# Optimization experiments

Hardware: AMD Instinct MI355X
Metric: run time of the kernel (lower is better)

Reference implementation:

```python
import jax, jax.numpy as jnp
import numpy as np

N = 100000      # nodes
E = 3200000     # edges (avg degree 32, undirected)
FIN = 256
FOUT = 256
K = 4


def setup_inputs() -> dict:
    key = jax.random.key(0)
    k1, k2, k3 = jax.random.split(key, 3)
    x = jax.random.normal(k1, (N, FIN), dtype=jnp.float32)
    edge_index = jax.random.randint(k2, (2, E), 0, N, dtype=jnp.int32)
    stdv = 1.0 / np.sqrt(FIN * K)
    # K per-hop dense projection weights, uniform(-stdv, stdv) as in reset_parameters
    weights = jax.random.uniform(k3, (K, FIN, FOUT), dtype=jnp.float32,
                                 minval=-stdv, maxval=stdv)
    return {"x": x, "edge_index": edge_index, "weights": weights}


def reference(x, edge_index, weights):
    # edge_index -> symmetric adjacency S (from_edgelist builds an undirected graph):
    # spmm(S, z)[i] = sum over neighbors j of z[j]; scatter-add both directions.
    src, dst = edge_index[0], edge_index[1]

    def spmm(z):
        out = jnp.zeros_like(z).at[dst].add(z[src])
        return out.at[src].add(z[dst])

    zs = [x]
    for _ in range(1, weights.shape[0]):
        x = spmm(x)           # [N, Fin] k-hop diffused features
        zs.append(x)
    # sum_k zs[k] @ weights[k]  -> [N, Fout]
    return jnp.einsum('knf,kfo->no', jnp.stack(zs), weights)
```

## Files before the change

kernel.cpp:

```cpp
#include <hip/hip_runtime.h>
#include <hip/hip_bf16.h>


#define NNODES 100000
#define NEDGES 3200000
#define FOUTF  256
#define MPAD   100096
#define MTILES 782
#define NB     782
#define NCHUNK 1024
#define CHUNK  3125

typedef __attribute__((ext_vector_type(4))) int   i32x4;
typedef __attribute__((ext_vector_type(4))) float f32x4;

__device__ __forceinline__ void async_ld16(const void* g, void* l) {
  __builtin_amdgcn_global_load_lds(
      (const __attribute__((address_space(1))) unsigned int*)g,
      (__attribute__((address_space(3))) unsigned int*)l, 16, 0, 0);
}


__global__ __launch_bounds__(256)
void chunk_count_kernel(const int* __restrict__ ei, int* __restrict__ cntg) {
  __shared__ int h[NB];
  for (int i = threadIdx.x; i < NB; i += 256) h[i] = 0;
  __syncthreads();
  const int e0 = blockIdx.x * CHUNK;
  const int e1 = (e0 + CHUNK < NEDGES) ? e0 + CHUNK : NEDGES;
  for (int e = e0 + threadIdx.x; e < e1; e += 256) {
    int s = ei[e];
    int d = ei[NEDGES + e];
    atomicAdd(&h[d >> 7], 1);
    atomicAdd(&h[s >> 7], 1);
  }
  __syncthreads();
  for (int i = threadIdx.x; i < NB; i += 256)
    cntg[blockIdx.x * NB + i] = h[i];
}

__global__ __launch_bounds__(256)
void scan_chunks_kernel(int* __restrict__ cntg, int* __restrict__ tot) {
  __shared__ int ws2[4];
  const int v = blockIdx.x;
  const int t = threadIdx.x, lane = t & 63, wv = t >> 6;
  int c[4];
  int sum = 0;
  #pragma unroll
  for (int i = 0; i < 4; ++i) { c[i] = cntg[(4 * t + i) * NB + v]; sum += c[i]; }
  int s = sum;
  #pragma unroll
  for (int off = 1; off < 64; off <<= 1) {
    int tmp = __shfl_up(s, off, 64);
    if (lane >= off) s += tmp;
  }
  if (lane == 63) ws2[wv] = s;
  __syncthreads();
  int wpre = 0;
  #pragma unroll
  for (int k = 0; k < 4; ++k) wpre += (k < wv) ? ws2[k] : 0;
  int run = wpre + s - sum;
  #pragma unroll
  for (int i = 0; i < 4; ++i) { int tmp = c[i]; cntg[(4 * t + i) * NB + v] = run; run += tmp; }
  if (t == 255) tot[v] = wpre + s;
}

__global__ __launch_bounds__(1024)
void base_scan_kernel(const int* __restrict__ tot, int* __restrict__ bbase) {
  __shared__ int ws[16];
  int t = threadIdx.x, lane = t & 63, wv = t >> 6;
  int v = (t < NB) ? tot[t] : 0;
  int s = v;
  #pragma unroll
  for (int off = 1; off < 64; off <<= 1) {
    int tmp = __shfl_up(s, off, 64);
    if (lane >= off) s += tmp;
  }
  if (lane == 63) ws[wv] = s;
  __syncthreads();
  if (t == 0) {
    int run = 0;
    #pragma unroll
    for (int k = 0; k < 16; ++k) { int tmp = ws[k]; ws[k] = run; run += tmp; }
  }
  __syncthreads();
  int excl = s + ws[wv] - v;
  if (t < NB) bbase[t] = excl;
  if (t == NB) bbase[NB] = excl;
}

__global__ __launch_bounds__(256)
void fill_kernel(const int* __restrict__ ei, const int* __restrict__ cntg,
                 const int* __restrict__ bbase, unsigned int* __restrict__ binned) {
  __shared__ int cur[NB];
  const int b = blockIdx.x;
  for (int i = threadIdx.x; i < NB; i += 256)
    cur[i] = bbase[i] + cntg[b * NB + i];
  __syncthreads();
  const int e0 = b * CHUNK;
  const int e1 = (e0 + CHUNK < NEDGES) ? e0 + CHUNK : NEDGES;
  for (int e = e0 + threadIdx.x; e < e1; e += 256) {
    int s = ei[e];
    int d = ei[NEDGES + e];
    int p = atomicAdd(&cur[d >> 7], 1);
    binned[p] = ((unsigned int)(d & 127) << 17) | (unsigned int)s;
    int q = atomicAdd(&cur[s >> 7], 1);
    binned[q] = ((unsigned int)(s & 127) << 17) | (unsigned int)d;
  }
}

__global__ __launch_bounds__(256)
void bucket_csr_kernel(const unsigned int* __restrict__ binned,
                       const int* __restrict__ bbase,
                       int* __restrict__ row_ptr, int* __restrict__ adj) {
  __shared__ int cnt[128];
  __shared__ int cur[128];
  const int b = blockIdx.x;
  const int node0 = b << 7;
  const int base = bbase[b];
  const int end = bbase[b + 1];
  const int tid = threadIdx.x;
  if (tid < 128) cnt[tid] = 0;
  __syncthreads();
  for (int i = base + tid; i < end; i += 256) {
    unsigned int v = binned[i];
    atomicAdd(&cnt[v >> 17], 1);
  }
  __syncthreads();
  if (tid < 128) {
    int ex = 0;
    #pragma unroll 8
    for (int j = 0; j < 128; ++j) {
      int c = cnt[j];
      ex += (j < tid) ? c : 0;
    }
    int node = node0 + tid;
    if (node < NNODES) row_ptr[node] = base + ex;
    cur[tid] = base + ex;
  }
  if (tid == 0 && b == NB - 1) row_ptr[NNODES] = end;
  __syncthreads();
  for (int i = base + tid; i < end; i += 256) {
    unsigned int v = binned[i];
    int nbr = (int)(v & 0x1FFFFu);
    int p = atomicAdd(&cur[v >> 17], 1);
    adj[p] = nbr << 8;
  }
}


__global__ __launch_bounds__(256)
void convert_x_kernel(const float* __restrict__ x,
                      unsigned char* __restrict__ g0,
                      float* __restrict__ sc0) {
  const int row = (blockIdx.x * 256 + threadIdx.x) >> 6;
  const int lane = threadIdx.x & 63;
  if (row >= NNODES) return;
  float4 xv = *(const float4*)&x[(size_t)row * 256 + (lane << 2)];

  float m = fmaxf(fmaxf(fabsf(xv.x), fabsf(xv.y)), fmaxf(fabsf(xv.z), fabsf(xv.w)));
  #pragma unroll
  for (int i = 1; i < 64; i <<= 1) m = fmaxf(m, __shfl_xor(m, i, 64));
  float inv = (m > 0.f) ? 127.f / m : 0.f;
  int q0 = (int)__builtin_rintf(xv.x * inv);
  int q1 = (int)__builtin_rintf(xv.y * inv);
  int q2 = (int)__builtin_rintf(xv.z * inv);
  int q3 = (int)__builtin_rintf(xv.w * inv);
  *(unsigned int*)(g0 + (size_t)row * 256 + (lane << 2)) =
      ((unsigned)q0 & 255u) | (((unsigned)q1 & 255u) << 8) |
      (((unsigned)q2 & 255u) << 16) | (((unsigned)q3 & 255u) << 24);
  if (lane == 0) sc0[row] = m * (1.f / 127.f);
}

__global__ __launch_bounds__(256)
void wmax_kernel(const float* __restrict__ w, unsigned int* __restrict__ dWmax) {
  __shared__ float red[4];
  const int k = blockIdx.x >> 6;
  const int chunk = blockIdx.x & 63;
  const float* wk = w + (size_t)k * 65536 + chunk * 1024;
  float m = 0.f;
  #pragma unroll
  for (int i = 0; i < 4; ++i) m = fmaxf(m, fabsf(wk[threadIdx.x + i * 256]));
  #pragma unroll
  for (int i = 1; i < 64; i <<= 1) m = fmaxf(m, __shfl_xor(m, i, 64));
  if ((threadIdx.x & 63) == 0) red[threadIdx.x >> 6] = m;
  __syncthreads();
  if (threadIdx.x == 0) {
    m = fmaxf(fmaxf(red[0], red[1]), fmaxf(red[2], red[3]));
    atomicMax(&dWmax[k], __float_as_uint(m));
  }
}

__global__ void quantw_kernel(const float* __restrict__ w,
                              const unsigned int* __restrict__ dWmax,
                              signed char* __restrict__ W8) {
  int idx = blockIdx.x * 256 + threadIdx.x;
  int k = idx >> 16, f = (idx >> 8) & 255, o = idx & 255;
  float mx = __uint_as_float(dWmax[k]);
  float inv = (mx > 0.f) ? 127.f / mx : 0.f;
  W8[(size_t)k * 65536 + o * 256 + f] = (signed char)(int)__builtin_rintf(w[idx] * inv);
}


#define DECQ(vv, ss)                                        \
  { acc0 += (ss) * (float)((vv) & 255u);                    \
    acc1 += (ss) * (float)(((vv) >> 8) & 255u);             \
    acc2 += (ss) * (float)(((vv) >> 16) & 255u);            \
    acc3 += (ss) * (float)((vv) >> 24);                     \
    ssum += (ss); }

__global__ __launch_bounds__(256)
void spmm_q8_kernel(const unsigned char* __restrict__ gin,
                    const float* __restrict__ sin,
                    unsigned char* __restrict__ gout,
                    float* __restrict__ sout,
                    const int* __restrict__ row_ptr,
                    const int* __restrict__ adjb) {
  const int wid = __builtin_amdgcn_readfirstlane((blockIdx.x * 256 + threadIdx.x) >> 6);
  const int lane = threadIdx.x & 63;
  if (wid >= NNODES) return;
  const int beg = row_ptr[wid];
  const int end = row_ptr[wid + 1];
  const int lb = lane << 2;
  const char* scb = (const char*)sin;

  float acc0 = 0.f, acc1 = 0.f, acc2 = 0.f, acc3 = 0.f, ssum = 0.f;
  int j = beg;
  for (; j + 4 <= end; j += 4) {
    int o0 = adjb[j + 0], o1 = adjb[j + 1], o2 = adjb[j + 2], o3 = adjb[j + 3];
    float s0 = *(const float*)(scb + (o0 >> 6));
    float s1 = *(const float*)(scb + (o1 >> 6));
    float s2 = *(const float*)(scb + (o2 >> 6));
    float s3 = *(const float*)(scb + (o3 >> 6));
    unsigned int v0 = *(const unsigned int*)(gin + o0 + lb) ^ 0x80808080u;
    unsigned int v1 = *(const unsigned int*)(gin + o1 + lb) ^ 0x80808080u;
    unsigned int v2 = *(const unsigned int*)(gin + o2 + lb) ^ 0x80808080u;
    unsigned int v3 = *(const unsigned int*)(gin + o3 + lb) ^ 0x80808080u;
    DECQ(v0, s0); DECQ(v1, s1); DECQ(v2, s2); DECQ(v3, s3);
  }
  for (; j < end; ++j) {
    int o = adjb[j];
    float s = *(const float*)(scb + (o >> 6));
    unsigned int v = *(const unsigned int*)(gin + o + lb) ^ 0x80808080u;
    DECQ(v, s);
  }

  const float bias = 128.f * ssum;
  const float a0 = acc0 - bias;
  const float a1 = acc1 - bias;
  const float a2 = acc2 - bias;
  const float a3 = acc3 - bias;

  float m = fmaxf(fmaxf(fabsf(a0), fabsf(a1)), fmaxf(fabsf(a2), fabsf(a3)));
  #pragma unroll
  for (int i = 1; i < 64; i <<= 1) m = fmaxf(m, __shfl_xor(m, i, 64));
  float inv = (m > 0.f) ? 127.f / m : 0.f;
  int q0 = (int)__builtin_rintf(a0 * inv);
  int q1 = (int)__builtin_rintf(a1 * inv);
  int q2 = (int)__builtin_rintf(a2 * inv);
  int q3 = (int)__builtin_rintf(a3 * inv);
  *(unsigned int*)(gout + (size_t)wid * 256 + lb) =
      ((unsigned)q0 & 255u) | (((unsigned)q1 & 255u) << 8) |
      (((unsigned)q2 & 255u) << 16) | (((unsigned)q3 & 255u) << 24);
  if (lane == 0) sout[wid] = m * (1.f / 127.f);
}


__global__ __launch_bounds__(512)
void gemm_i8_kernel(const unsigned char* __restrict__ q0p,
                    const unsigned char* __restrict__ q1p,
                    const unsigned char* __restrict__ q2p,
                    const unsigned char* __restrict__ q3p,
                    const float* __restrict__ s0p,
                    const float* __restrict__ s1p,
                    const float* __restrict__ s2p,
                    const float* __restrict__ s3p,
                    const signed char* __restrict__ W8,
                    const unsigned int* __restrict__ dWmax,
                    float* __restrict__ C) {
  __shared__ __align__(16) unsigned char smem[49152];
  unsigned char* As = smem;
  unsigned char* Bs = smem + 16384;
  const int tid = threadIdx.x;
  const int lane = tid & 63;
  const int wave = tid >> 6;
  const int wr = wave >> 2;
  const int wc = wave & 3;
  const int rowA_base = blockIdx.x * 128;

  const unsigned char* qs[4] = {q0p, q1p, q2p, q3p};
  const float* scs[4] = {s0p, s1p, s2p, s3p};

  f32x4 accf[4][4] = {};

  #pragma unroll
  for (int k = 0; k < 4; ++k) {
    const unsigned char* Qk = qs[k];
    const signed char* Wk = W8 + (size_t)k * 65536;
    i32x4 acci[4][4] = {};
    #pragma unroll
    for (int kc = 0; kc < 2; ++kc) {
      __syncthreads();
      #pragma unroll
      for (int i = 0; i < 2; ++i) {
        int slot = tid + 512 * i;
        int row = slot >> 3;
        int col = ((slot & 7) << 4) ^ ((row & 7) << 4);
        async_ld16(Qk + (size_t)(rowA_base + row) * 256 + kc * 128 + col,
                   &As[slot * 16]);
      }
      #pragma unroll
      for (int i = 0; i < 4; ++i) {
        int slot = tid + 512 * i;
        int row = slot >> 3;
        int col = ((slot & 7) << 4) ^ ((row & 7) << 4);
        async_ld16(Wk + (size_t)row * 256 + kc * 128 + col, &Bs[slot * 16]);
      }
      __syncthreads();
      #pragma unroll
      for (int kk = 0; kk < 2; ++kk) {
        const int kb = kk * 64 + ((lane >> 4) << 4);
        i32x4 a[4], b[4];
        #pragma unroll
        for (int m = 0; m < 4; ++m) {
          int row = wr * 64 + m * 16 + (lane & 15);
          a[m] = *(const i32x4*)&As[row * 128 + (kb ^ ((row & 7) << 4))];
        }
        #pragma unroll
        for (int n = 0; n < 4; ++n) {
          int row = wc * 64 + n * 16 + (lane & 15);
          b[n] = *(const i32x4*)&Bs[row * 128 + (kb ^ ((row & 7) << 4))];
        }
        #pragma unroll
        for (int m = 0; m < 4; ++m) {
          #pragma unroll
          for (int n = 0; n < 4; ++n)
            acci[m][n] = __builtin_amdgcn_mfma_i32_16x16x64_i8(a[m], b[n], acci[m][n], 0, 0, 0);
        }
      }
    }
    const float dWk = __uint_as_float(dWmax[k]) * (1.f / 127.f);
    const float* sk = scs[k];
    #pragma unroll
    for (int m = 0; m < 4; ++m) {
      #pragma unroll
      for (int j = 0; j < 4; ++j) {
        int r = rowA_base + wr * 64 + ((lane >> 4) << 2) + m * 16 + j;
        float s = sk[r] * dWk;
        #pragma unroll
        for (int n = 0; n < 4; ++n)
          accf[m][n][j] += s * (float)acci[m][n][j];
      }
    }
  }

  __syncthreads();
  float* myCs = (float*)smem + wave * 1056;
  #pragma unroll
  for (int m = 0; m < 4; ++m) {
    #pragma unroll
    for (int n = 0; n < 4; ++n) {
      #pragma unroll
      for (int j = 0; j < 4; ++j)
        myCs[(((lane >> 4) << 2) | j) * 66 + (lane & 15) + n * 16] = accf[m][n][j];
    }
    #pragma unroll
    for (int it = 0; it < 4; ++it) {
      int row = it * 4 + (lane >> 4);
      f32x4 v = *(const f32x4*)&myCs[row * 66 + ((lane & 15) << 2)];
      int r = rowA_base + wr * 64 + m * 16 + row;
      if (r < NNODES)
        *(f32x4*)&C[(size_t)r * FOUTF + wc * 64 + ((lane & 15) << 2)] = v;
    }
  }
}


extern "C" void kernel_launch(void* const* d_in, const int* in_sizes, int n_in,
                              void* d_out, int out_size, void* d_ws, size_t ws_size,
                              hipStream_t stream) {
  (void)in_sizes; (void)n_in; (void)out_size; (void)ws_size;
  const float* x  = (const float*)d_in[0];
  const int*   ei = (const int*)d_in[1];
  const float* w  = (const float*)d_in[2];
  float* out = (float*)d_out;

  char* ws = (char*)d_ws;
  size_t off = 0;
  auto carve = [&](size_t bytes) -> void* {
    void* p = ws + off;
    off = (off + bytes + 255) & ~(size_t)255;
    return p;
  };
  unsigned char* gA = (unsigned char*)carve((size_t)MPAD * 256);
  unsigned char* gB = (unsigned char*)carve((size_t)MPAD * 256);
  unsigned char* gC = (unsigned char*)carve((size_t)MPAD * 256);
  unsigned char* gD = (unsigned char*)carve((size_t)MPAD * 256);
  float* scA        = (float*)carve((size_t)MPAD * 4);
  float* scB        = (float*)carve((size_t)MPAD * 4);
  float* scC        = (float*)carve((size_t)MPAD * 4);
  float* scD        = (float*)carve((size_t)MPAD * 4);
  signed char* W8   = (signed char*)carve((size_t)4 * 65536);
  unsigned int* dWmax = (unsigned int*)carve(4 * 4);
  int* row_ptr      = (int*)carve((size_t)(NNODES + 1) * 4);
  int* adj          = (int*)carve((size_t)2 * NEDGES * 4);
  int* cntg         = (int*)carve((size_t)NCHUNK * NB * 4);
  int* tot          = (int*)carve((size_t)NB * 4);
  int* bbase        = (int*)carve((size_t)(NB + 1) * 4);
  unsigned int* binned = (unsigned int*)gD;

  hipMemsetAsync(dWmax, 0, 16, stream);

  chunk_count_kernel<<<NCHUNK, 256, 0, stream>>>(ei, cntg);
  scan_chunks_kernel<<<NB, 256, 0, stream>>>(cntg, tot);
  base_scan_kernel<<<1, 1024, 0, stream>>>(tot, bbase);
  fill_kernel<<<NCHUNK, 256, 0, stream>>>(ei, cntg, bbase, binned);
  bucket_csr_kernel<<<NB, 256, 0, stream>>>(binned, bbase, row_ptr, adj);

  convert_x_kernel<<<25000, 256, 0, stream>>>(x, gA, scA);
  wmax_kernel<<<256, 256, 0, stream>>>(w, dWmax);
  quantw_kernel<<<1024, 256, 0, stream>>>(w, dWmax, W8);

  spmm_q8_kernel<<<25000, 256, 0, stream>>>(gA, scA, gB, scB, row_ptr, adj);
  spmm_q8_kernel<<<25000, 256, 0, stream>>>(gB, scB, gC, scC, row_ptr, adj);
  spmm_q8_kernel<<<25000, 256, 0, stream>>>(gC, scC, gD, scD, row_ptr, adj);

  gemm_i8_kernel<<<MTILES, 512, 0, stream>>>(gA, gB, gC, gD, scA, scB, scC, scD,
                                             W8, dWmax, out);
}
```

Baseline: 938.9 us.

## Fuse front kernels, sort adjacency per row, use persistent spmm grid

Merges x quantization, edge chunk counting and weight max reduction into one launch with block-range dispatch. Adds a per-row sort of adjacency entries by high bits of the byte offset so neighbor gathers walk memory in coarse order. Switches the spmm kernels to a grid-stride persistent layout of 2048 blocks. Together these aim to cut launch overhead and improve gather locality, at the cost of an extra sort pass over the adjacency.

```diff
diff --git a/kernel.cpp b/kernel.cpp
--- a/kernel.cpp
+++ b/kernel.cpp
@@ -20,24 +20,63 @@
       (__attribute__((address_space(3))) unsigned int*)l, 16, 0, 0);
 }
 
-
-__global__ __launch_bounds__(256)
-void chunk_count_kernel(const int* __restrict__ ei, int* __restrict__ cntg) {
+__global__ __launch_bounds__(256)
+void front_kernel(const float* __restrict__ x,
+                  unsigned char* __restrict__ g0, float* __restrict__ sc0,
+                  const int* __restrict__ ei, int* __restrict__ cntg,
+                  const float* __restrict__ w, unsigned int* __restrict__ dWmax) {
   __shared__ int h[NB];
-  for (int i = threadIdx.x; i < NB; i += 256) h[i] = 0;
-  __syncthreads();
-  const int e0 = blockIdx.x * CHUNK;
-  const int e1 = (e0 + CHUNK < NEDGES) ? e0 + CHUNK : NEDGES;
-  for (int e = e0 + threadIdx.x; e < e1; e += 256) {
-    int s = ei[e];
-    int d = ei[NEDGES + e];
-    atomicAdd(&h[d >> 7], 1);
-    atomicAdd(&h[s >> 7], 1);
-  }
-  __syncthreads();
-  for (int i = threadIdx.x; i < NB; i += 256)
-    cntg[blockIdx.x * NB + i] = h[i];
-}
+  const int bid = blockIdx.x;
+  if (bid < 25000) {
+    const int row = (bid * 256 + threadIdx.x) >> 6;
+    const int lane = threadIdx.x & 63;
+    if (row >= NNODES) return;
+    float4 xv = *(const float4*)&x[(size_t)row * 256 + (lane << 2)];
+    float m = fmaxf(fmaxf(fabsf(xv.x), fabsf(xv.y)), fmaxf(fabsf(xv.z), fabsf(xv.w)));
+    #pragma unroll
+    for (int i = 1; i < 64; i <<= 1) m = fmaxf(m, __shfl_xor(m, i, 64));
+    float inv = (m > 0.f) ? 127.f / m : 0.f;
+    int q0 = (int)__builtin_rintf(xv.x * inv);
+    int q1 = (int)__builtin_rintf(xv.y * inv);
+    int q2 = (int)__builtin_rintf(xv.z * inv);
+    int q3 = (int)__builtin_rintf(xv.w * inv);
+    *(unsigned int*)(g0 + (size_t)row * 256 + (lane << 2)) =
+        ((unsigned)q0 & 255u) | (((unsigned)q1 & 255u) << 8) |
+        (((unsigned)q2 & 255u) << 16) | (((unsigned)q3 & 255u) << 24);
+    if (lane == 0) sc0[row] = m * (1.f / 127.f);
+  } else if (bid < 26024) {
+    const int b = bid - 25000;
+    for (int i = threadIdx.x; i < NB; i += 256) h[i] = 0;
+    __syncthreads();
+    const int e0 = b * CHUNK;
+    const int e1 = (e0 + CHUNK < NEDGES) ? e0 + CHUNK : NEDGES;
+    for (int e = e0 + threadIdx.x; e < e1; e += 256) {
+      int s = ei[e];
+      int d = ei[NEDGES + e];
+      atomicAdd(&h[d >> 7], 1);
+      atomicAdd(&h[s >> 7], 1);
+    }
+    __syncthreads();
+    for (int i = threadIdx.x; i < NB; i += 256)
+      cntg[b * NB + i] = h[i];
+  } else {
+    const int b = bid - 26024;
+    const int k = b >> 6;
+    const int chunk = b & 63;
+    const float* wk = w + (size_t)k * 65536 + chunk * 1024;
+    float m = 0.f;
+    #pragma unroll
+    for (int i = 0; i < 4; ++i) m = fmaxf(m, fabsf(wk[threadIdx.x + i * 256]));
+    #pragma unroll
+    for (int i = 1; i < 64; i <<= 1) m = fmaxf(m, __shfl_xor(m, i, 64));
+    if (threadIdx.x == 0) h[0] = 0;
+    __syncthreads();
+    if ((threadIdx.x & 63) == 0) atomicMax(&h[0], __float_as_int(m));
+    __syncthreads();
+    if (threadIdx.x == 0) atomicMax(&dWmax[k], (unsigned int)h[0]);
+  }
+}
+
 
 __global__ __launch_bounds__(256)
 void scan_chunks_kernel(int* __restrict__ cntg, int* __restrict__ tot) {
@@ -148,46 +187,43 @@
   }
 }
 
-
-__global__ __launch_bounds__(256)
-void convert_x_kernel(const float* __restrict__ x,
-                      unsigned char* __restrict__ g0,
-                      float* __restrict__ sc0) {
-  const int row = (blockIdx.x * 256 + threadIdx.x) >> 6;
+__global__ __launch_bounds__(256)
+void sort_adj_kernel(const int* __restrict__ row_ptr, int* __restrict__ adj) {
+  __shared__ int cnt[4][32];
+  __shared__ int cur[4][32];
+  const int wv = threadIdx.x >> 6;
   const int lane = threadIdx.x & 63;
-  if (row >= NNODES) return;
-  float4 xv = *(const float4*)&x[(size_t)row * 256 + (lane << 2)];
-
-  float m = fmaxf(fmaxf(fabsf(xv.x), fabsf(xv.y)), fmaxf(fabsf(xv.z), fabsf(xv.w)));
-  #pragma unroll
-  for (int i = 1; i < 64; i <<= 1) m = fmaxf(m, __shfl_xor(m, i, 64));
-  float inv = (m > 0.f) ? 127.f / m : 0.f;
-  int q0 = (int)__builtin_rintf(xv.x * inv);
-  int q1 = (int)__builtin_rintf(xv.y * inv);
-  int q2 = (int)__builtin_rintf(xv.z * inv);
-  int q3 = (int)__builtin_rintf(xv.w * inv);
-  *(unsigned int*)(g0 + (size_t)row * 256 + (lane << 2)) =
-      ((unsigned)q0 & 255u) | (((unsigned)q1 & 255u) << 8) |
-      (((unsigned)q2 & 255u) << 16) | (((unsigned)q3 & 255u) << 24);
-  if (lane == 0) sc0[row] = m * (1.f / 127.f);
-}
-
-__global__ __launch_bounds__(256)
-void wmax_kernel(const float* __restrict__ w, unsigned int* __restrict__ dWmax) {
-  __shared__ float red[4];
-  const int k = blockIdx.x >> 6;
-  const int chunk = blockIdx.x & 63;
-  const float* wk = w + (size_t)k * 65536 + chunk * 1024;
-  float m = 0.f;
-  #pragma unroll
-  for (int i = 0; i < 4; ++i) m = fmaxf(m, fabsf(wk[threadIdx.x + i * 256]));
-  #pragma unroll
-  for (int i = 1; i < 64; i <<= 1) m = fmaxf(m, __shfl_xor(m, i, 64));
-  if ((threadIdx.x & 63) == 0) red[threadIdx.x >> 6] = m;
-  __syncthreads();
-  if (threadIdx.x == 0) {
-    m = fmaxf(fmaxf(red[0], red[1]), fmaxf(red[2], red[3]));
-    atomicMax(&dWmax[k], __float_as_uint(m));
+  const int wid = blockIdx.x * 4 + wv;
+  if (wid >= NNODES) return;
+  const int beg = row_ptr[wid];
+  const int deg = row_ptr[wid + 1] - beg;
+  if (deg > 256) return;
+  if (lane < 32) cnt[wv][lane] = 0;
+  int v[4];
+  #pragma unroll
+  for (int i = 0; i < 4; ++i) {
+    int idx = lane + 64 * i;
+    v[i] = (idx < deg) ? adj[beg + idx] : -1;
+  }
+  #pragma unroll
+  for (int i = 0; i < 4; ++i)
+    if (v[i] >= 0) atomicAdd(&cnt[wv][((unsigned)v[i]) >> 20], 1);
+  if (lane < 32) {
+    int c = cnt[wv][lane];
+    int s = c;
+    #pragma unroll
+    for (int off = 1; off < 32; off <<= 1) {
+      int tmp = __shfl_up(s, off, 32);
+      if ((lane & 31) >= off) s += tmp;
+    }
+    cur[wv][lane] = s - c;
+  }
+  #pragma unroll
+  for (int i = 0; i < 4; ++i) {
+    if (v[i] >= 0) {
+      int pos = atomicAdd(&cur[wv][((unsigned)v[i]) >> 20], 1);
+      adj[beg + pos] = v[i];
+    }
   }
 }
 
@@ -216,53 +252,57 @@
                     float* __restrict__ sout,
                     const int* __restrict__ row_ptr,
                     const int* __restrict__ adjb) {
-  const int wid = __builtin_amdgcn_readfirstlane((blockIdx.x * 256 + threadIdx.x) >> 6);
+  const int wv = threadIdx.x >> 6;
   const int lane = threadIdx.x & 63;
-  if (wid >= NNODES) return;
-  const int beg = row_ptr[wid];
-  const int end = row_ptr[wid + 1];
+  const int wbase = blockIdx.x * 4 + wv;
   const int lb = lane << 2;
   const char* scb = (const char*)sin;
 
-  float acc0 = 0.f, acc1 = 0.f, acc2 = 0.f, acc3 = 0.f, ssum = 0.f;
-  int j = beg;
-  for (; j + 4 <= end; j += 4) {
-    int o0 = adjb[j + 0], o1 = adjb[j + 1], o2 = adjb[j + 2], o3 = adjb[j + 3];
-    float s0 = *(const float*)(scb + (o0 >> 6));
-    float s1 = *(const float*)(scb + (o1 >> 6));
-    float s2 = *(const float*)(scb + (o2 >> 6));
-    float s3 = *(const float*)(scb + (o3 >> 6));
-    unsigned int v0 = *(const unsigned int*)(gin + o0 + lb) ^ 0x80808080u;
-    unsigned int v1 = *(const unsigned int*)(gin + o1 + lb) ^ 0x80808080u;
-    unsigned int v2 = *(const unsigned int*)(gin + o2 + lb) ^ 0x80808080u;
-    unsigned int v3 = *(const unsigned int*)(gin + o3 + lb) ^ 0x80808080u;
-    DECQ(v0, s0); DECQ(v1, s1); DECQ(v2, s2); DECQ(v3, s3);
-  }
-  for (; j < end; ++j) {
-    int o = adjb[j];
-    float s = *(const float*)(scb + (o >> 6));
-    unsigned int v = *(const unsigned int*)(gin + o + lb) ^ 0x80808080u;
-    DECQ(v, s);
-  }
-
-  const float bias = 128.f * ssum;
-  const float a0 = acc0 - bias;
-  const float a1 = acc1 - bias;
-  const float a2 = acc2 - bias;
-  const float a3 = acc3 - bias;
-
-  float m = fmaxf(fmaxf(fabsf(a0), fabsf(a1)), fmaxf(fabsf(a2), fabsf(a3)));
-  #pragma unroll
-  for (int i = 1; i < 64; i <<= 1) m = fmaxf(m, __shfl_xor(m, i, 64));
-  float inv = (m > 0.f) ? 127.f / m : 0.f;
-  int q0 = (int)__builtin_rintf(a0 * inv);
-  int q1 = (int)__builtin_rintf(a1 * inv);
-  int q2 = (int)__builtin_rintf(a2 * inv);
-  int q3 = (int)__builtin_rintf(a3 * inv);
-  *(unsigned int*)(gout + (size_t)wid * 256 + lb) =
-      ((unsigned)q0 & 255u) | (((unsigned)q1 & 255u) << 8) |
-      (((unsigned)q2 & 255u) << 16) | (((unsigned)q3 & 255u) << 24);
-  if (lane == 0) sout[wid] = m * (1.f / 127.f);
+  for (int wid0 = wbase; wid0 < NNODES; wid0 += 8192) {
+    const int wid = __builtin_amdgcn_readfirstlane(wid0);
+    const int beg = row_ptr[wid];
+    const int end = row_ptr[wid + 1];
+
+    float acc0 = 0.f, acc1 = 0.f, acc2 = 0.f, acc3 = 0.f, ssum = 0.f;
+    int j = beg;
+    for (; j + 4 <= end; j += 4) {
+      int o0 = adjb[j + 0], o1 = adjb[j + 1], o2 = adjb[j + 2], o3 = adjb[j + 3];
+      float s0 = *(const float*)(scb + (o0 >> 6));
+      float s1 = *(const float*)(scb + (o1 >> 6));
+      float s2 = *(const float*)(scb + (o2 >> 6));
+      float s3 = *(const float*)(scb + (o3 >> 6));
+      unsigned int v0 = *(const unsigned int*)(gin + o0 + lb) ^ 0x80808080u;
+      unsigned int v1 = *(const unsigned int*)(gin + o1 + lb) ^ 0x80808080u;
+      unsigned int v2 = *(const unsigned int*)(gin + o2 + lb) ^ 0x80808080u;
+      unsigned int v3 = *(const unsigned int*)(gin + o3 + lb) ^ 0x80808080u;
+      DECQ(v0, s0); DECQ(v1, s1); DECQ(v2, s2); DECQ(v3, s3);
+    }
+    for (; j < end; ++j) {
+      int o = adjb[j];
+      float s = *(const float*)(scb + (o >> 6));
+      unsigned int v = *(const unsigned int*)(gin + o + lb) ^ 0x80808080u;
+      DECQ(v, s);
+    }
+
+    const float bias = 128.f * ssum;
+    const float a0 = acc0 - bias;
+    const float a1 = acc1 - bias;
+    const float a2 = acc2 - bias;
+    const float a3 = acc3 - bias;
+
+    float m = fmaxf(fmaxf(fabsf(a0), fabsf(a1)), fmaxf(fabsf(a2), fabsf(a3)));
+    #pragma unroll
+    for (int i = 1; i < 64; i <<= 1) m = fmaxf(m, __shfl_xor(m, i, 64));
+    float inv = (m > 0.f) ? 127.f / m : 0.f;
+    int q0 = (int)__builtin_rintf(a0 * inv);
+    int q1 = (int)__builtin_rintf(a1 * inv);
+    int q2 = (int)__builtin_rintf(a2 * inv);
+    int q3 = (int)__builtin_rintf(a3 * inv);
+    *(unsigned int*)(gout + (size_t)wid * 256 + lb) =
+        ((unsigned)q0 & 255u) | (((unsigned)q1 & 255u) << 8) |
+        (((unsigned)q2 & 255u) << 16) | (((unsigned)q3 & 255u) << 24);
+    if (lane == 0) sout[wid] = m * (1.f / 127.f);
+  }
 }
 
 
@@ -411,19 +451,17 @@
 
   hipMemsetAsync(dWmax, 0, 16, stream);
 
-  chunk_count_kernel<<<NCHUNK, 256, 0, stream>>>(ei, cntg);
+  front_kernel<<<26280, 256, 0, stream>>>(x, gA, scA, ei, cntg, w, dWmax);
   scan_chunks_kernel<<<NB, 256, 0, stream>>>(cntg, tot);
   base_scan_kernel<<<1, 1024, 0, stream>>>(tot, bbase);
   fill_kernel<<<NCHUNK, 256, 0, stream>>>(ei, cntg, bbase, binned);
   bucket_csr_kernel<<<NB, 256, 0, stream>>>(binned, bbase, row_ptr, adj);
-
-  convert_x_kernel<<<25000, 256, 0, stream>>>(x, gA, scA);
-  wmax_kernel<<<256, 256, 0, stream>>>(w, dWmax);
+  sort_adj_kernel<<<25000, 256, 0, stream>>>(row_ptr, adj);
   quantw_kernel<<<1024, 256, 0, stream>>>(w, dWmax, W8);
 
-  spmm_q8_kernel<<<25000, 256, 0, stream>>>(gA, scA, gB, scB, row_ptr, adj);
-  spmm_q8_kernel<<<25000, 256, 0, stream>>>(gB, scB, gC, scC, row_ptr, adj);
-  spmm_q8_kernel<<<25000, 256, 0, stream>>>(gC, scC, gD, scD, row_ptr, adj);
+  spmm_q8_kernel<<<2048, 256, 0, stream>>>(gA, scA, gB, scB, row_ptr, adj);
+  spmm_q8_kernel<<<2048, 256, 0, stream>>>(gB, scB, gC, scC, row_ptr, adj);
+  spmm_q8_kernel<<<2048, 256, 0, stream>>>(gC, scC, gD, scD, row_ptr, adj);
 
   gemm_i8_kernel<<<MTILES, 512, 0, stream>>>(gA, gB, gC, gD, scA, scB, scC, scD,
                                              W8, dWmax, out);
```

After: 1.005 ms. +7.1%, slower.
